# Kernel tuning notes

Measured on AMD Instinct MI355X. Metric: run time of the kernel, lower is better.

## Reference

```python
import jax, jax.numpy as jnp
import numpy as np

D_MODEL = 768
D_STATE = 16
D_CONV = 4
EXPAND = 2
D_INNER = D_MODEL * EXPAND  # 1536
B = 2
T = 8192
ALPHA = 0.9  # hard-coded EMA coefficient in _parallel_scan


def setup_inputs() -> dict:
    key = jax.random.key(0)
    ks = jax.random.split(key, 12)
    s = 0.02
    return {
        "x": jax.random.normal(ks[0], (B, T, D_MODEL), jnp.float32),
        "in_w": jax.random.normal(ks[1], (D_MODEL, 2 * D_INNER), jnp.float32) * s,
        "in_b": jnp.zeros((2 * D_INNER,), jnp.float32),
        "conv_w": jax.random.normal(ks[2], (D_INNER, 1, D_CONV), jnp.float32) * s,  # OIH, depthwise
        "conv_b": jnp.zeros((D_INNER,), jnp.float32),
        "xp_w": jax.random.normal(ks[3], (D_INNER, 2 * D_STATE), jnp.float32) * s,
        "xp_b": jnp.zeros((2 * D_STATE,), jnp.float32),
        "dt_w": jax.random.normal(ks[4], (D_STATE, D_INNER), jnp.float32) * s,
        "dt_b": jnp.zeros((D_INNER,), jnp.float32),
        "D_param": jnp.ones((D_INNER,), jnp.float32),
        "out_w": jax.random.normal(ks[5], (D_INNER, D_MODEL), jnp.float32) * s,
        "out_b": jnp.zeros((D_MODEL,), jnp.float32),
    }


def _forward(x, in_w, in_b, conv_w, conv_b, xp_w, xp_b, dt_w, dt_b, D_param, out_w, out_b):
    # in_proj: [B,T,D] -> [B,T,2*d_inner]
    xz = x @ in_w + in_b
    x_inner, z = jnp.split(xz, 2, axis=-1)

    # Causal depthwise conv1d (torch pads both sides by d_conv-1 then slices [:T],
    # which is equivalent to left-pad d_conv-1, right-pad 0)
    xc = jnp.transpose(x_inner, (0, 2, 1))  # [B, d_inner, T]
    xc = jax.lax.conv_general_dilated(
        xc, conv_w, window_strides=(1,), padding=[(D_CONV - 1, 0)],
        dimension_numbers=("NCH", "OIH", "NCH"), feature_group_count=D_INNER,
    ) + conv_b[None, :, None]
    x_conv = jax.nn.silu(jnp.transpose(xc, (0, 2, 1)))  # [B, T, d_inner]

    # NOTE: original computes x_proj/dt_proj/A_bar here, but _parallel_scan ignores
    # A_bar/B_ssm/C_ssm entirely, so they are dead code w.r.t. the output (omitted).

    # Serial EMA scan: h_t = alpha*h_{t-1} + (1-alpha)*x_conv_t
    def step(h, xt):
        h = ALPHA * h + (1.0 - ALPHA) * xt
        return h, h

    h0 = jnp.zeros((x.shape[0], D_INNER), x_conv.dtype)
    _, hs = jax.lax.scan(step, h0, jnp.transpose(x_conv, (1, 0, 2)))  # [T,B,d_inner]
    scan_out = jnp.transpose(hs, (1, 0, 2))

    y = x_conv * D_param + scan_out
    y = y * jax.nn.silu(z)
    return y @ out_w + out_b  # dropout is identity at inference


def reference(x, in_w, in_b, conv_w, conv_b, xp_w, xp_b, dt_w, dt_b, D_param, out_w, out_b):
    return _forward(x, in_w, in_b, conv_w, conv_b, xp_w, xp_b, dt_w, dt_b, D_param, out_w, out_b)
```

## Files before the change

kernel.cpp:

```cpp
#include <hip/hip_runtime.h>

#define D_MODEL 768
#define D_INNER 1536
#define NXZ     3072
#define BATCH   2
#define SEQ     8192
#define MTOT    (BATCH*SEQ)
#define WARM    64

typedef _Float16 v8h __attribute__((ext_vector_type(8)));
typedef _Float16 v4h __attribute__((ext_vector_type(4)));
typedef float    v4f __attribute__((ext_vector_type(4)));
typedef _Float16 f16;

__device__ __forceinline__ float frcp(float x) {
  float r;
  asm volatile("v_rcp_f32 %0, %1" : "=v"(r) : "v"(x));
  return r;
}
__device__ __forceinline__ float fsilu(float u) {
  return u * frcp(1.f + __expf(-u));
}

#define NCVT (MTOT * D_MODEL / 4 / 256)
#define NT1  ((NXZ / 32) * (D_MODEL / 32))
#define NT2  ((D_MODEL / 32) * (D_INNER / 32))

__device__ __forceinline__ void transpose_tile(const float* __restrict__ in,
                                               f16* __restrict__ out,
                                               int R, int C, int bx, int by, int tid) {
  __shared__ float tile[32][33];
  const int c0 = bx * 32, r0 = by * 32;
  const int tx = tid & 31, ty = tid >> 5;
#pragma unroll
  for (int i = 0; i < 32; i += 8)
    tile[ty + i][tx] = in[(long)(r0 + ty + i) * C + (c0 + tx)];
  __syncthreads();
#pragma unroll
  for (int i = 0; i < 32; i += 8)
    out[(long)(c0 + ty + i) * R + (r0 + tx)] = (f16)tile[tx][ty + i];
}

__global__ void k_prep(const float* __restrict__ x, f16* __restrict__ xb,
                       const float* __restrict__ in_w, f16* __restrict__ wInT,
                       const float* __restrict__ out_w, f16* __restrict__ wOutT) {
  const int bid = blockIdx.x;
  const int tid = threadIdx.x;
  if (bid < NCVT) {
    const int i = bid * 256 + tid;
    float4 v = reinterpret_cast<const float4*>(x)[i];
    v4h o;
    o[0] = (f16)v.x; o[1] = (f16)v.y; o[2] = (f16)v.z; o[3] = (f16)v.w;
    reinterpret_cast<v4h*>(xb)[i] = o;
  } else if (bid < NCVT + NT1) {
    const int b2 = bid - NCVT;
    transpose_tile(in_w, wInT, D_MODEL, NXZ, b2 % (NXZ / 32), b2 / (NXZ / 32), tid);
  } else {
    const int b2 = bid - NCVT - NT1;
    transpose_tile(out_w, wOutT, D_INNER, D_MODEL, b2 % (D_MODEL / 32), b2 / (D_MODEL / 32), tid);
  }
}

__device__ __forceinline__ void gload_lds16(const void* g, void* l) {
  __builtin_amdgcn_global_load_lds((const __attribute__((address_space(1))) void*)g,
                                   (__attribute__((address_space(3))) void*)l, 16, 0, 0);
}

template <bool F16OUT>
__launch_bounds__(256, 2)
__global__ void k_gemm_bt(const f16* __restrict__ A, const f16* __restrict__ Bt,
                          const float* __restrict__ bias, void* __restrict__ Cv,
                          int M, int N, int K) {
  __shared__ f16 As[128][64];
  __shared__ f16 Bs[128][64];
  const int tid  = threadIdx.x;
  const int lane = tid & 63;
  const int wave = tid >> 6;
  const int wm   = (wave >> 1) * 64;
  const int wn   = (wave & 1) * 64;
  const int m16  = lane & 15;
  const int quad = lane >> 4;
  const long m0 = (long)blockIdx.y * 128;
  const long n0 = (long)blockIdx.x * 128;

  v4f acc[4][4];
#pragma unroll
  for (int i = 0; i < 4; i++)
#pragma unroll
    for (int j = 0; j < 4; j++)
#pragma unroll
      for (int r = 0; r < 4; r++) acc[i][j][r] = 0.f;

  const int  srow = wave * 8 + (lane >> 3);
  const int  gcol = ((lane & 7) ^ (lane >> 3)) << 3;
  const f16* Ag = A  + (m0 + srow) * (long)K + gcol;
  const f16* Bg = Bt + (n0 + srow) * (long)K + gcol;

  const int c0q = ((quad ^ (m16 & 7)) << 3);
  const int c1q = c0q ^ 32;

  for (int k0 = 0; k0 < K; k0 += 64) {
#pragma unroll
    for (int g = 0; g < 4; ++g) {
      gload_lds16(Ag + (long)(g * 32) * K, &As[wave * 8 + g * 32][0]);
      gload_lds16(Bg + (long)(g * 32) * K, &Bs[wave * 8 + g * 32][0]);
    }
    Ag += 64; Bg += 64;
    __syncthreads();
    v8h af[4], bfr[4];
#pragma unroll
    for (int i = 0; i < 4; i++) af[i]  = *(const v8h*)&As[wm + i * 16 + m16][c0q];
#pragma unroll
    for (int j = 0; j < 4; j++) bfr[j] = *(const v8h*)&Bs[wn + j * 16 + m16][c0q];
#pragma unroll
    for (int i = 0; i < 4; i++)
#pragma unroll
      for (int j = 0; j < 4; j++)
        acc[i][j] = __builtin_amdgcn_mfma_f32_16x16x32_f16(af[i], bfr[j], acc[i][j], 0, 0, 0);
#pragma unroll
    for (int i = 0; i < 4; i++) af[i]  = *(const v8h*)&As[wm + i * 16 + m16][c1q];
#pragma unroll
    for (int j = 0; j < 4; j++) bfr[j] = *(const v8h*)&Bs[wn + j * 16 + m16][c1q];
#pragma unroll
    for (int i = 0; i < 4; i++)
#pragma unroll
      for (int j = 0; j < 4; j++)
        acc[i][j] = __builtin_amdgcn_mfma_f32_16x16x32_f16(af[i], bfr[j], acc[i][j], 0, 0, 0);
    __syncthreads();
  }

#pragma unroll
  for (int i = 0; i < 4; i++) {
#pragma unroll
    for (int j = 0; j < 4; j++) {
      const long n = n0 + wn + j * 16 + m16;
      const float bv = bias[n];
#pragma unroll
      for (int r = 0; r < 4; r++) {
        const long m = m0 + wm + i * 16 + quad * 4 + r;
        float v = acc[i][j][r] + bv;
        if (F16OUT) ((f16*)Cv)[m * N + n] = (f16)v;
        else        ((float*)Cv)[m * N + n] = v;
      }
    }
  }
}

template <bool F16OUT>
__launch_bounds__(256, 2)
__global__ void k_gemm_big(const f16* __restrict__ A, const f16* __restrict__ Bt,
                           const float* __restrict__ bias, void* __restrict__ Cv,
                           int M, int N, int K) {
  __shared__ f16 As[256][64];
  __shared__ f16 Bs[128][64];
  const int tid  = threadIdx.x;
  const int lane = tid & 63;
  const int wave = tid >> 6;
  const int wm   = (wave >> 1) * 128;
  const int wn   = (wave & 1) * 64;
  const int m16  = lane & 15;
  const int quad = lane >> 4;
  const long m0 = (long)blockIdx.y * 256;
  const long n0 = (long)blockIdx.x * 128;

  v4f acc[8][4];
#pragma unroll
  for (int i = 0; i < 8; i++)
#pragma unroll
    for (int j = 0; j < 4; j++)
#pragma unroll
      for (int r = 0; r < 4; r++) acc[i][j][r] = 0.f;

  const int  srow = wave * 8 + (lane >> 3);
  const int  gcol = ((lane & 7) ^ (lane >> 3)) << 3;
  const f16* Ag = A  + (m0 + srow) * (long)K + gcol;
  const f16* Bg = Bt + (n0 + srow) * (long)K + gcol;
  f16* AsW = &As[wave * 8][0];
  f16* BsW = &Bs[wave * 8][0];

  const int c0q = ((quad ^ (m16 & 7)) << 3);
  const int c1q = c0q ^ 32;

  for (int k0 = 0; k0 < K; k0 += 64) {
#pragma unroll
    for (int g = 0; g < 8; ++g)
      gload_lds16(Ag + (long)(g * 32) * K, AsW + g * 32 * 64);
#pragma unroll
    for (int g = 0; g < 4; ++g)
      gload_lds16(Bg + (long)(g * 32) * K, BsW + g * 32 * 64);
    Ag += 64; Bg += 64;
    __syncthreads();
    v8h bfr[4], af;
#pragma unroll
    for (int j = 0; j < 4; j++) bfr[j] = *(const v8h*)&Bs[wn + j * 16 + m16][c0q];
#pragma unroll
    for (int i = 0; i < 8; i++) {
      af = *(const v8h*)&As[wm + i * 16 + m16][c0q];
#pragma unroll
      for (int j = 0; j < 4; j++)
        acc[i][j] = __builtin_amdgcn_mfma_f32_16x16x32_f16(af, bfr[j], acc[i][j], 0, 0, 0);
    }
#pragma unroll
    for (int j = 0; j < 4; j++) bfr[j] = *(const v8h*)&Bs[wn + j * 16 + m16][c1q];
#pragma unroll
    for (int i = 0; i < 8; i++) {
      af = *(const v8h*)&As[wm + i * 16 + m16][c1q];
#pragma unroll
      for (int j = 0; j < 4; j++)
        acc[i][j] = __builtin_amdgcn_mfma_f32_16x16x32_f16(af, bfr[j], acc[i][j], 0, 0, 0);
    }
    __syncthreads();
  }

#pragma unroll
  for (int i = 0; i < 8; i++) {
#pragma unroll
    for (int j = 0; j < 4; j++) {
      const long n = n0 + wn + j * 16 + m16;
      const float bv = bias[n];
#pragma unroll
      for (int r = 0; r < 4; r++) {
        const long m = m0 + wm + i * 16 + quad * 4 + r;
        float v = acc[i][j][r] + bv;
        if (F16OUT) ((f16*)Cv)[m * N + n] = (f16)v;
        else        ((float*)Cv)[m * N + n] = v;
      }
    }
  }
}

__launch_bounds__(256, 4)
__global__ void k_conv_scan(const f16* __restrict__ xz, const float* __restrict__ conv_w,
                            const float* __restrict__ conv_b, const float* __restrict__ Dp_,
                            f16* __restrict__ y) {
  const int tid = threadIdx.x;
  const int c   = blockIdx.y * 256 + tid;
  const int b   = blockIdx.z;
  const int t0  = blockIdx.x * 64;
  const float w0 = conv_w[c * 4 + 0], w1 = conv_w[c * 4 + 1];
  const float w2 = conv_w[c * 4 + 2], w3 = conv_w[c * 4 + 3];
  const float cb = conv_b[c], Dp = Dp_[c];
  const long mb = (long)b * SEQ;

  const f16* xcol = xz + mb * (long)NXZ + c;
  const f16* zcol = xcol + D_INNER;
  f16*       ycol = y  + mb * (long)D_INNER + c;

  float xm3 = 0.f, xm2 = 0.f, xm1 = 0.f, h = 0.f;
  int ts = t0 - WARM;
  if (t0 > 0) {
    xm3 = (float)xcol[(long)(ts - 3) * NXZ];
    xm2 = (float)xcol[(long)(ts - 2) * NXZ];
    xm1 = (float)xcol[(long)(ts - 1) * NXZ];
  } else {
    ts = 0;
  }

#pragma unroll 8
  for (int t = ts; t < t0; ++t) {
    float xt = (float)xcol[(long)t * NXZ];
    float u  = w0 * xm3 + w1 * xm2 + w2 * xm1 + w3 * xt + cb;
    h = 0.9f * h + 0.1f * fsilu(u);
    xm3 = xm2; xm2 = xm1; xm1 = xt;
  }
#pragma unroll 8
  for (int t = t0; t < t0 + 64; ++t) {
    float xt = (float)xcol[(long)t * NXZ];
    float zv = (float)zcol[(long)t * NXZ];
    float u  = w0 * xm3 + w1 * xm2 + w2 * xm1 + w3 * xt + cb;
    float v  = fsilu(u);
    h = 0.9f * h + 0.1f * v;
    ycol[(long)t * D_INNER] = (f16)((v * Dp + h) * fsilu(zv));
    xm3 = xm2; xm2 = xm1; xm1 = xt;
  }
}

extern "C" void kernel_launch(void* const* d_in, const int* in_sizes, int n_in,
                              void* d_out, int out_size, void* d_ws, size_t ws_size,
                              hipStream_t stream) {
  const float* x       = (const float*)d_in[0];
  const float* in_w    = (const float*)d_in[1];
  const float* in_b    = (const float*)d_in[2];
  const float* conv_w  = (const float*)d_in[3];
  const float* conv_b  = (const float*)d_in[4];
  const float* D_param = (const float*)d_in[9];
  const float* out_w   = (const float*)d_in[10];
  const float* out_b   = (const float*)d_in[11];
  float* out = (float*)d_out;

  char* p = (char*)d_ws;
  f16* xb    = (f16*)p; p += (size_t)MTOT * D_MODEL * 2;
  f16* wInT  = (f16*)p; p += (size_t)NXZ * D_MODEL * 2;
  f16* wOutT = (f16*)p; p += (size_t)D_MODEL * D_INNER * 2;
  f16* xzb   = (f16*)p; p += (size_t)MTOT * NXZ * 2;
  f16* yb    = (f16*)p; p += (size_t)MTOT * D_INNER * 2;

  k_prep<<<NCVT + NT1 + NT2, 256, 0, stream>>>(x, xb, in_w, wInT, out_w, wOutT);

  k_gemm_bt<true><<<dim3(NXZ / 128, MTOT / 128), 256, 0, stream>>>(xb, wInT, in_b, xzb, MTOT, NXZ, D_MODEL);

  k_conv_scan<<<dim3(SEQ / 64, D_INNER / 256, BATCH), 256, 0, stream>>>(xzb, conv_w, conv_b, D_param, yb);

  k_gemm_big<false><<<dim3(D_MODEL / 128, MTOT / 256), 256, 0, stream>>>(yb, wOutT, out_b, out, MTOT, D_MODEL, D_INNER);
}
```

Measured before the change: 324.4 us.

## Store in_proj output channel-major so the conv-scan reads time-contiguous vectors

The first GEMM's epilogue now writes xz transposed, with channels as rows and time contiguous, using 4-wide f16 stores. The conv+EMA scan kernel then loads 8 consecutive timesteps per thread with a single 16-byte load, instead of one strided scalar load per timestep. This cuts load instruction count and latency stalls in the serial scan loop. The trade-off is that threads in a wave now touch different rows, so access is uncoalesced across lanes, and the GEMM stores are scattered across many rows.

```diff
diff --git a/kernel.cpp b/kernel.cpp
--- a/kernel.cpp
+++ b/kernel.cpp
@@ -66,11 +66,10 @@
                                    (__attribute__((address_space(3))) void*)l, 16, 0, 0);
 }
 
-template <bool F16OUT>
 __launch_bounds__(256, 2)
-__global__ void k_gemm_bt(const f16* __restrict__ A, const f16* __restrict__ Bt,
-                          const float* __restrict__ bias, void* __restrict__ Cv,
-                          int M, int N, int K) {
+__global__ void k_gemm_bt_T(const f16* __restrict__ A, const f16* __restrict__ Bt,
+                            const float* __restrict__ bias, f16* __restrict__ CT,
+                            int M, int N, int K) {
   __shared__ f16 As[128][64];
   __shared__ f16 Bs[128][64];
   const int tid  = threadIdx.x;
@@ -131,17 +130,15 @@
 
 #pragma unroll
   for (int i = 0; i < 4; i++) {
+    const long mB = m0 + wm + i * 16 + quad * 4;
 #pragma unroll
     for (int j = 0; j < 4; j++) {
       const long n = n0 + wn + j * 16 + m16;
       const float bv = bias[n];
-#pragma unroll
-      for (int r = 0; r < 4; r++) {
-        const long m = m0 + wm + i * 16 + quad * 4 + r;
-        float v = acc[i][j][r] + bv;
-        if (F16OUT) ((f16*)Cv)[m * N + n] = (f16)v;
-        else        ((float*)Cv)[m * N + n] = v;
-      }
+      v4h o;
+#pragma unroll
+      for (int r = 0; r < 4; r++) o[r] = (f16)(acc[i][j][r] + bv);
+      *(v4h*)&CT[n * (long)M + mB] = o;
     }
   }
 }
@@ -230,7 +227,7 @@
 }
 
 __launch_bounds__(256, 4)
-__global__ void k_conv_scan(const f16* __restrict__ xz, const float* __restrict__ conv_w,
+__global__ void k_conv_scan(const f16* __restrict__ xzT, const float* __restrict__ conv_w,
                             const float* __restrict__ conv_b, const float* __restrict__ Dp_,
                             f16* __restrict__ y) {
   const int tid = threadIdx.x;
@@ -242,36 +239,43 @@
   const float cb = conv_b[c], Dp = Dp_[c];
   const long mb = (long)b * SEQ;
 
-  const f16* xcol = xz + mb * (long)NXZ + c;
-  const f16* zcol = xcol + D_INNER;
-  f16*       ycol = y  + mb * (long)D_INNER + c;
+  const f16* xr = xzT + (long)c * MTOT + mb;
+  const f16* zr = xzT + (long)(D_INNER + c) * MTOT + mb;
+  f16*       yc = y + (mb + t0) * (long)D_INNER + c;
 
   float xm3 = 0.f, xm2 = 0.f, xm1 = 0.f, h = 0.f;
-  int ts = t0 - WARM;
+  const int ts = t0 - WARM;
   if (t0 > 0) {
-    xm3 = (float)xcol[(long)(ts - 3) * NXZ];
-    xm2 = (float)xcol[(long)(ts - 2) * NXZ];
-    xm1 = (float)xcol[(long)(ts - 1) * NXZ];
-  } else {
-    ts = 0;
-  }
-
-#pragma unroll 8
-  for (int t = ts; t < t0; ++t) {
-    float xt = (float)xcol[(long)t * NXZ];
-    float u  = w0 * xm3 + w1 * xm2 + w2 * xm1 + w3 * xt + cb;
-    h = 0.9f * h + 0.1f * fsilu(u);
-    xm3 = xm2; xm2 = xm1; xm1 = xt;
-  }
-#pragma unroll 8
-  for (int t = t0; t < t0 + 64; ++t) {
-    float xt = (float)xcol[(long)t * NXZ];
-    float zv = (float)zcol[(long)t * NXZ];
-    float u  = w0 * xm3 + w1 * xm2 + w2 * xm1 + w3 * xt + cb;
-    float v  = fsilu(u);
-    h = 0.9f * h + 0.1f * v;
-    ycol[(long)t * D_INNER] = (f16)((v * Dp + h) * fsilu(zv));
-    xm3 = xm2; xm2 = xm1; xm1 = xt;
+    xm3 = (float)xr[ts - 3];
+    xm2 = (float)xr[ts - 2];
+    xm1 = (float)xr[ts - 1];
+#pragma unroll 1
+    for (int tb = 0; tb < 8; ++tb) {
+      const v8h xv = *(const v8h*)&xr[ts + tb * 8];
+#pragma unroll
+      for (int e = 0; e < 8; ++e) {
+        float xt = (float)xv[e];
+        float u  = w0 * xm3 + w1 * xm2 + w2 * xm1 + w3 * xt + cb;
+        h = 0.9f * h + 0.1f * fsilu(u);
+        xm3 = xm2; xm2 = xm1; xm1 = xt;
+      }
+    }
+  }
+
+#pragma unroll 1
+  for (int tb = 0; tb < 8; ++tb) {
+    const v8h xv = *(const v8h*)&xr[t0 + tb * 8];
+    const v8h zv = *(const v8h*)&zr[t0 + tb * 8];
+#pragma unroll
+    for (int e = 0; e < 8; ++e) {
+      float xt = (float)xv[e];
+      float u  = w0 * xm3 + w1 * xm2 + w2 * xm1 + w3 * xt + cb;
+      float v  = fsilu(u);
+      h = 0.9f * h + 0.1f * v;
+      float g  = fsilu((float)zv[e]);
+      yc[(long)(tb * 8 + e) * D_INNER] = (f16)((v * Dp + h) * g);
+      xm3 = xm2; xm2 = xm1; xm1 = xt;
+    }
   }
 }
 
@@ -292,14 +296,14 @@
   f16* xb    = (f16*)p; p += (size_t)MTOT * D_MODEL * 2;
   f16* wInT  = (f16*)p; p += (size_t)NXZ * D_MODEL * 2;
   f16* wOutT = (f16*)p; p += (size_t)D_MODEL * D_INNER * 2;
-  f16* xzb   = (f16*)p; p += (size_t)MTOT * NXZ * 2;
+  f16* xzT   = (f16*)p; p += (size_t)NXZ * MTOT * 2;
   f16* yb    = (f16*)p; p += (size_t)MTOT * D_INNER * 2;
 
   k_prep<<<NCVT + NT1 + NT2, 256, 0, stream>>>(x, xb, in_w, wInT, out_w, wOutT);
 
-  k_gemm_bt<true><<<dim3(NXZ / 128, MTOT / 128), 256, 0, stream>>>(xb, wInT, in_b, xzb, MTOT, NXZ, D_MODEL);
-
-  k_conv_scan<<<dim3(SEQ / 64, D_INNER / 256, BATCH), 256, 0, stream>>>(xzb, conv_w, conv_b, D_param, yb);
+  k_gemm_bt_T<<<dim3(NXZ / 128, MTOT / 128), 256, 0, stream>>>(xb, wInT, in_b, xzT, MTOT, NXZ, D_MODEL);
+
+  k_conv_scan<<<dim3(SEQ / 64, D_INNER / 256, BATCH), 256, 0, stream>>>(xzT, conv_w, conv_b, D_param, yb);
 
   k_gemm_big<false><<<dim3(D_MODEL / 128, MTOT / 256), 256, 0, stream>>>(yb, wOutT, out_b, out, MTOT, D_MODEL, D_INNER);
 }
```

After: 445.2 us. +37.2%, slower.
